# Optimization experiments

Measured on AMD Instinct MI355X. Metric: run time of the kernel, lower is better.

The kernel has to match this reference:

```python
import jax, jax.numpy as jnp
import numpy as np

D_FEAT, HID, N_LAYERS = 6, 64, 2
NEG_SLOPE = 0.01


def gru_layer(x_seq, W_ih, W_hh, b_ih, b_hh):
    # x_seq: [T, N, in]; PyTorch gate order r, z, n
    N = x_seq.shape[1]
    h0 = jnp.zeros((N, W_hh.shape[1]), x_seq.dtype)
    def step(h, x_t):
        gi = x_t @ W_ih.T + b_ih
        gh = h @ W_hh.T + b_hh
        i_r, i_z, i_n = jnp.split(gi, 3, axis=-1)
        h_r, h_z, h_n = jnp.split(gh, 3, axis=-1)
        r = jax.nn.sigmoid(i_r + h_r)
        z = jax.nn.sigmoid(i_z + h_z)
        n = jnp.tanh(i_n + r * h_n)
        h_new = (1.0 - z) * n + z * h
        return h_new, h_new
    _, ys = jax.lax.scan(step, h0, x_seq)
    return ys  # [T, N, H]


def setup_inputs() -> dict:
    key = jax.random.key(0)
    ks = jax.random.split(key, 16)
    N, T = 4000, 60
    x = jax.random.normal(ks[0], (N, D_FEAT * T), dtype=jnp.float32)
    relation_matrix = jax.random.randint(ks[1], (N, N, 8), 0, 2).astype(jnp.float32)
    s = 0.1
    p = {
        'W_ih0': jax.random.normal(ks[2], (3 * HID, D_FEAT), jnp.float32) * s,
        'W_hh0': jax.random.normal(ks[3], (3 * HID, HID), jnp.float32) * s,
        'b_ih0': jnp.zeros((3 * HID,), jnp.float32),
        'b_hh0': jnp.zeros((3 * HID,), jnp.float32),
        'W_ih1': jax.random.normal(ks[4], (3 * HID, HID), jnp.float32) * s,
        'W_hh1': jax.random.normal(ks[5], (3 * HID, HID), jnp.float32) * s,
        'b_ih1': jnp.zeros((3 * HID,), jnp.float32),
        'b_hh1': jnp.zeros((3 * HID,), jnp.float32),
        'W_0': jax.random.normal(ks[6], (2 * HID, 1), jnp.float32) * s,
        'b_0': jnp.zeros((), jnp.float32),
        'W_1': jax.random.normal(ks[7], (2 * HID, 1), jnp.float32) * s,
        'b_1': jnp.zeros((), jnp.float32),
        'W_2': jax.random.normal(ks[8], (2 * HID, 1), jnp.float32) * s,
        'b_2': jnp.zeros((), jnp.float32),
        'fc_w': jax.random.normal(ks[9], (1, 2 * HID), jnp.float32) * s,
        'fc_b': jnp.zeros((1,), jnp.float32),
    }
    return dict(x=x, relation_matrix=relation_matrix, **p)


def _head_softmax(h, W, b, mask):
    # weight[i,j] = leaky_relu(h_i @ W[:H] + h_j @ W[H:] + b); avoids [N,N,2H] concat
    H = h.shape[1]
    a = h @ W[:H]            # [N,1]
    c = h @ W[H:]            # [N,1]
    w = jax.nn.leaky_relu(a + c.T + b, NEG_SLOPE)  # [N,N]
    valid = jnp.where(mask == 0, -1000000.0, mask * w)
    return jax.nn.softmax(valid, axis=1)


def reference(x, relation_matrix, W_ih0, W_hh0, b_ih0, b_hh0, W_ih1, W_hh1, b_ih1, b_hh1,
              W_0, b_0, W_1, b_1, W_2, b_2, fc_w, fc_b):
    N = x.shape[0]
    xs = x.reshape(N, D_FEAT, -1).transpose(2, 0, 1)  # [T, N, d_feat]
    y1 = gru_layer(xs, W_ih0, W_hh0, b_ih0, b_hh0)
    y2 = gru_layer(y1, W_ih1, W_hh1, b_ih1, b_hh1)
    h = y2[-1]  # [N, H] last time step
    mask = jnp.sum(relation_matrix, axis=2)  # [N, N]
    s0 = _head_softmax(h, W_0, b_0, mask)
    s1 = _head_softmax(h, W_1, b_1, mask)
    s2 = _head_softmax(h, W_2, b_2, mask)
    agg = ((s0 + s1 + s2) / 3.0) @ h  # [N, H]
    hid = jnp.concatenate([h, agg], axis=1)  # [N, 2H]
    pred = (hid @ fc_w.T + fc_b).squeeze(-1)  # [N]
    return pred
```

## Files before the change

### kernel.cpp

```cpp
#include <hip/hip_runtime.h>

typedef __attribute__((ext_vector_type(8))) short bf16x8;
typedef __attribute__((ext_vector_type(4))) float f32x4;
typedef __attribute__((ext_vector_type(4))) float f4v;

__device__ __forceinline__ unsigned short f2bf(float f){
  unsigned u = __builtin_bit_cast(unsigned, f);
  u += 0x7FFFu + ((u >> 16) & 1u);
  return (unsigned short)(u >> 16);
}
__device__ __forceinline__ float bf2f(unsigned short b){
  unsigned u = ((unsigned)b) << 16;
  return __builtin_bit_cast(float, u);
}
__device__ __forceinline__ float sigmoidf_(float x){ return 1.f/(1.f + __expf(-x)); }
__device__ __forceinline__ float tanhf_(float x){
  float a = fabsf(x);
  float t = __expf(-2.f*a);
  float r = (1.f - t)/(1.f + t);
  return copysignf(r, x);
}

struct WF { bf16x8 hi, lo; };

__device__ __forceinline__ void mmsplit(bf16x8 ah, bf16x8 al, const WF& B,
                                        f32x4& Dh, f32x4& Dl){
  Dh = __builtin_amdgcn_mfma_f32_16x16x32_bf16(ah, B.hi, Dh, 0, 0, 0);
  Dl = __builtin_amdgcn_mfma_f32_16x16x32_bf16(al, B.hi, Dl, 0, 0, 0);
  Dl = __builtin_amdgcn_mfma_f32_16x16x32_bf16(ah, B.lo, Dl, 0, 0, 0);
}

__device__ __forceinline__ WF load_wf(const float* W, int ldk, int row, int k0, int kmax){
  WF f;
  #pragma unroll
  for (int j = 0; j < 8; j++){
    int k = k0 + j;
    float v = (k < kmax) ? W[row*ldk + k] : 0.f;
    unsigned short hb = f2bf(v);
    f.hi[j] = (short)hb;
    f.lo[j] = (short)f2bf(v - bf2f(hb));
  }
  return f;
}

__global__ __launch_bounds__(256, 1)
void gru_kernel(const float* __restrict__ x,
                const float* __restrict__ Wih0, const float* __restrict__ Whh0,
                const float* __restrict__ bih0, const float* __restrict__ bhh0,
                const float* __restrict__ Wih1, const float* __restrict__ Whh1,
                const float* __restrict__ bih1, const float* __restrict__ bhh1,
                float* __restrict__ hfin){
  __shared__ unsigned short xp_hi[16][60][8];
  __shared__ unsigned short xp_lo[16][60][8];
  __shared__ unsigned short h0hi[2][16][72], h0lo[2][16][72];
  __shared__ unsigned short h1hi[2][16][72], h1lo[2][16][72];

  const int tid  = threadIdx.x;
  const int lane = tid & 63;
  const int w    = tid >> 6;
  const int c    = lane & 15;
  const int q    = lane >> 4;
  const int d    = w*16 + c;
  const int nbase = blockIdx.x * 16;

  for (int v = tid; v < 16*360; v += 256){
    int n = v / 360, rem = v % 360;
    int dd = rem / 60, tt = rem % 60;
    float f = x[(size_t)(nbase + n)*360 + rem];
    unsigned short hb = f2bf(f);
    xp_hi[n][tt][dd] = hb;
    xp_lo[n][tt][dd] = f2bf(f - bf2f(hb));
  }
  for (int v = tid; v < 16*60*2; v += 256){
    int n = v / 120, rem = v % 120;
    int tt = rem >> 1, dd = 6 + (rem & 1);
    xp_hi[n][tt][dd] = 0; xp_lo[n][tt][dd] = 0;
  }
  for (int v = tid; v < 2*16*72; v += 256){
    ((unsigned short*)h0hi)[v] = 0; ((unsigned short*)h0lo)[v] = 0;
    ((unsigned short*)h1hi)[v] = 0; ((unsigned short*)h1lo)[v] = 0;
  }

  const float bi0r = bih0[d], bi0z = bih0[64+d], bi0n = bih0[128+d];
  const float bh0r = bhh0[d], bh0z = bhh0[64+d], bh0n = bhh0[128+d];
  const float bi1r = bih1[d], bi1z = bih1[64+d], bi1n = bih1[128+d];
  const float bh1r = bhh1[d], bh1z = bhh1[64+d], bh1n = bhh1[128+d];

  WF Bih0[3];
  WF Bhh0[3][2], Bih1[3][2], Bhh1[3][2];
  #pragma unroll
  for (int g = 0; g < 3; g++){
    int row = g*64 + d;
    Bih0[g] = load_wf(Wih0, 6, row, q*8, 6);
    #pragma unroll
    for (int kt = 0; kt < 2; kt++){
      Bhh0[g][kt] = load_wf(Whh0, 64, row, kt*32 + q*8, 64);
      Bih1[g][kt] = load_wf(Wih1, 64, row, kt*32 + q*8, 64);
      Bhh1[g][kt] = load_wf(Whh1, 64, row, kt*32 + q*8, 64);
    }
  }

  float h0old[4] = {0,0,0,0}, h1old[4] = {0,0,0,0};

  __syncthreads();

  #pragma unroll 1
  for (int t = 0; t < 60; t++){
    const int p  = t & 1;
    const int qb = p ^ 1;

    bf16x8 a_h0h[2], a_h0l[2];
    #pragma unroll
    for (int kt = 0; kt < 2; kt++){
      a_h0h[kt] = *(const bf16x8*)&h0hi[p][c][kt*32 + q*8];
      a_h0l[kt] = *(const bf16x8*)&h0lo[p][c][kt*32 + q*8];
    }
    bf16x8 a_xh = {}, a_xl = {};
    if (q == 0){
      a_xh = *(const bf16x8*)&xp_hi[c][t][0];
      a_xl = *(const bf16x8*)&xp_lo[c][t][0];
    }

    f32x4 RH = {0,0,0,0}, RL = {0,0,0,0};
    f32x4 ZH = {0,0,0,0}, ZL = {0,0,0,0};
    f32x4 NIH = {0,0,0,0}, NIL = {0,0,0,0};
    f32x4 NHH = {0,0,0,0}, NHL = {0,0,0,0};
    mmsplit(a_xh, a_xl, Bih0[0], RH, RL);
    mmsplit(a_xh, a_xl, Bih0[1], ZH, ZL);
    mmsplit(a_xh, a_xl, Bih0[2], NIH, NIL);
    #pragma unroll
    for (int kt = 0; kt < 2; kt++){
      mmsplit(a_h0h[kt], a_h0l[kt], Bhh0[0][kt], RH, RL);
      mmsplit(a_h0h[kt], a_h0l[kt], Bhh0[1][kt], ZH, ZL);
      mmsplit(a_h0h[kt], a_h0l[kt], Bhh0[2][kt], NHH, NHL);
    }
    #pragma unroll
    for (int rI = 0; rI < 4; rI++){
      float rv = sigmoidf_(RH[rI] + RL[rI] + bi0r + bh0r);
      float zv = sigmoidf_(ZH[rI] + ZL[rI] + bi0z + bh0z);
      float nv = tanhf_(NIH[rI] + NIL[rI] + bi0n + rv*(NHH[rI] + NHL[rI] + bh0n));
      float hnew = (1.f - zv)*nv + zv*h0old[rI];
      h0old[rI] = hnew;
      unsigned short hb = f2bf(hnew);
      int node = q*4 + rI;
      h0hi[qb][node][d] = hb;
      h0lo[qb][node][d] = f2bf(hnew - bf2f(hb));
    }
    __syncthreads();

    bf16x8 a_yh[2], a_yl[2], a_h1h[2], a_h1l[2];
    #pragma unroll
    for (int kt = 0; kt < 2; kt++){
      a_yh[kt]  = *(const bf16x8*)&h0hi[qb][c][kt*32 + q*8];
      a_yl[kt]  = *(const bf16x8*)&h0lo[qb][c][kt*32 + q*8];
      a_h1h[kt] = *(const bf16x8*)&h1hi[p][c][kt*32 + q*8];
      a_h1l[kt] = *(const bf16x8*)&h1lo[p][c][kt*32 + q*8];
    }
    f32x4 EH = {0,0,0,0}, EL = {0,0,0,0};
    f32x4 FH = {0,0,0,0}, FL = {0,0,0,0};
    f32x4 GIH = {0,0,0,0}, GIL = {0,0,0,0};
    f32x4 GHH = {0,0,0,0}, GHL = {0,0,0,0};
    #pragma unroll
    for (int kt = 0; kt < 2; kt++){
      mmsplit(a_yh[kt], a_yl[kt], Bih1[0][kt], EH, EL);
      mmsplit(a_yh[kt], a_yl[kt], Bih1[1][kt], FH, FL);
      mmsplit(a_yh[kt], a_yl[kt], Bih1[2][kt], GIH, GIL);
      mmsplit(a_h1h[kt], a_h1l[kt], Bhh1[0][kt], EH, EL);
      mmsplit(a_h1h[kt], a_h1l[kt], Bhh1[1][kt], FH, FL);
      mmsplit(a_h1h[kt], a_h1l[kt], Bhh1[2][kt], GHH, GHL);
    }
    #pragma unroll
    for (int rI = 0; rI < 4; rI++){
      float rv = sigmoidf_(EH[rI] + EL[rI] + bi1r + bh1r);
      float zv = sigmoidf_(FH[rI] + FL[rI] + bi1z + bh1z);
      float nv = tanhf_(GIH[rI] + GIL[rI] + bi1n + rv*(GHH[rI] + GHL[rI] + bh1n));
      float hnew = (1.f - zv)*nv + zv*h1old[rI];
      h1old[rI] = hnew;
      unsigned short hb = f2bf(hnew);
      int node = q*4 + rI;
      h1hi[qb][node][d] = hb;
      h1lo[qb][node][d] = f2bf(hnew - bf2f(hb));
    }
  }

  #pragma unroll
  for (int rI = 0; rI < 4; rI++){
    int node = nbase + q*4 + rI;
    hfin[(size_t)node*64 + d] = h1old[rI];
  }
}

__global__ void ac_kernel(const float* __restrict__ hfin,
                          const float* __restrict__ W0h, const float* __restrict__ W1h,
                          const float* __restrict__ W2h, float* __restrict__ ac){
  int lane = threadIdx.x & 63;
  int node = blockIdx.x*4 + (threadIdx.x >> 6);
  float hv = hfin[(size_t)node*64 + lane];
  const float* Ws[3] = {W0h, W1h, W2h};
  #pragma unroll
  for (int h = 0; h < 3; h++){
    float pa = hv * Ws[h][lane];
    float pc = hv * Ws[h][64 + lane];
    #pragma unroll
    for (int m = 32; m >= 1; m >>= 1){
      pa += __shfl_xor(pa, m, 64);
      pc += __shfl_xor(pc, m, 64);
    }
    if (lane == 0){
      ac[(size_t)(2*h)*4000 + node]   = pa;
      ac[(size_t)(2*h+1)*4000 + node] = pc;
    }
  }
}

__global__ __launch_bounds__(256, 3)
void attn2_kernel(const float* __restrict__ rel, const float* __restrict__ hfin,
                  const float* __restrict__ ac,
                  const float* __restrict__ b0p, const float* __restrict__ b1p,
                  const float* __restrict__ b2p,
                  const float* __restrict__ fcw, const float* __restrict__ fcb,
                  float* __restrict__ pred){
  __shared__ float m0[4000], m1[4000];
  __shared__ float red[4][8];

  const int tid  = threadIdx.x;
  const int lane = tid & 63;
  const int w    = tid >> 6;
  const int i0   = blockIdx.x * 2;
  const float bh[3] = {b0p[0], b1p[0], b2p[0]};

  const float* c0 = ac + 1*4000;
  const float* c1 = ac + 3*4000;
  const float* c2 = ac + 5*4000;

  float ai[2][3];
  #pragma unroll
  for (int r = 0; r < 2; r++)
    #pragma unroll
    for (int h = 0; h < 3; h++)
      ai[r][h] = ac[(size_t)(2*h)*4000 + i0 + r];

  float z[2][3] = {{0.f,0.f,0.f},{0.f,0.f,0.f}};

  {
    int j = tid;
    bool have = (j < 4000);
    f4v r0, r1, r2, r3;
    if (have){
      const f4v* rp0 = (const f4v*)(rel + ((size_t)i0*4000 + j)*8);
      const f4v* rp1 = (const f4v*)(rel + ((size_t)(i0+1)*4000 + j)*8);
      r0 = __builtin_nontemporal_load(rp0);
      r1 = __builtin_nontemporal_load(rp0 + 1);
      r2 = __builtin_nontemporal_load(rp1);
      r3 = __builtin_nontemporal_load(rp1 + 1);
    }
    while (have){
      int jn = j + 256;
      bool haven = (jn < 4000);
      f4v n0, n1, n2, n3;
      if (haven){
        const f4v* rp0 = (const f4v*)(rel + ((size_t)i0*4000 + jn)*8);
        const f4v* rp1 = (const f4v*)(rel + ((size_t)(i0+1)*4000 + jn)*8);
        n0 = __builtin_nontemporal_load(rp0);
        n1 = __builtin_nontemporal_load(rp0 + 1);
        n2 = __builtin_nontemporal_load(rp1);
        n3 = __builtin_nontemporal_load(rp1 + 1);
      }
      float mk0 = r0[0]+r0[1]+r0[2]+r0[3] + r1[0]+r1[1]+r1[2]+r1[3];
      float mk1 = r2[0]+r2[1]+r2[2]+r2[3] + r3[0]+r3[1]+r3[2]+r3[3];
      m0[j] = mk0; m1[j] = mk1;
      float cv[3] = {c0[j], c1[j], c2[j]};
      #pragma unroll
      for (int h = 0; h < 3; h++){
        float s0 = ai[0][h] + cv[h] + bh[h];
        float s1 = ai[1][h] + cv[h] + bh[h];
        float w0 = s0 > 0.f ? s0 : 0.01f*s0;
        float w1 = s1 > 0.f ? s1 : 0.01f*s1;
        float v0 = (mk0 == 0.f) ? -1e6f : mk0*w0;
        float v1 = (mk1 == 0.f) ? -1e6f : mk1*w1;
        z[0][h] += __expf(v0);
        z[1][h] += __expf(v1);
      }
      r0 = n0; r1 = n1; r2 = n2; r3 = n3;
      j = jn; have = haven;
    }
  }
  #pragma unroll
  for (int r = 0; r < 2; r++)
    #pragma unroll
    for (int h = 0; h < 3; h++){
      float v = z[r][h];
      #pragma unroll
      for (int m = 32; m >= 1; m >>= 1) v += __shfl_xor(v, m, 64);
      if (lane == 0) red[w][r*3 + h] = v;
    }
  __syncthreads();
  float iZ[2][3];
  #pragma unroll
  for (int r = 0; r < 2; r++)
    #pragma unroll
    for (int h = 0; h < 3; h++)
      iZ[r][h] = 1.f/(red[0][r*3+h] + red[1][r*3+h] + red[2][r*3+h] + red[3][r*3+h]);

  for (int j = tid; j < 4000; j += 256){
    float mk0 = m0[j], mk1 = m1[j];
    float cv[3] = {c0[j], c1[j], c2[j]};
    float w0s = 0.f, w1s = 0.f;
    #pragma unroll
    for (int h = 0; h < 3; h++){
      float s0 = ai[0][h] + cv[h] + bh[h];
      float s1 = ai[1][h] + cv[h] + bh[h];
      float w0 = s0 > 0.f ? s0 : 0.01f*s0;
      float w1 = s1 > 0.f ? s1 : 0.01f*s1;
      float v0 = (mk0 == 0.f) ? -1e6f : mk0*w0;
      float v1 = (mk1 == 0.f) ? -1e6f : mk1*w1;
      w0s += __expf(v0) * iZ[0][h];
      w1s += __expf(v1) * iZ[1][h];
    }
    m0[j] = w0s * (1.f/3.f);
    m1[j] = w1s * (1.f/3.f);
  }
  __syncthreads();

  float acc0 = 0.f, acc1 = 0.f;
  const int jb = w * 1000;
  for (int jj = 0; jj < 1000; jj += 4){
    float4 w0 = *(const float4*)&m0[jb + jj];
    float4 w1 = *(const float4*)&m1[jb + jj];
    float w0a[4] = {w0.x, w0.y, w0.z, w0.w};
    float w1a[4] = {w1.x, w1.y, w1.z, w1.w};
    #pragma unroll
    for (int k = 0; k < 4; k++){
      float hv = hfin[(size_t)(jb + jj + k)*64 + lane];
      acc0 = fmaf(w0a[k], hv, acc0);
      acc1 = fmaf(w1a[k], hv, acc1);
    }
  }
  __syncthreads();
  m0[(w*2 + 0)*64 + lane] = acc0;
  m0[(w*2 + 1)*64 + lane] = acc1;
  __syncthreads();
  if (tid < 128){
    int r = tid >> 6, d = tid & 63;
    float agg = m0[(0*2+r)*64 + d] + m0[(1*2+r)*64 + d]
              + m0[(2*2+r)*64 + d] + m0[(3*2+r)*64 + d];
    float term = hfin[(size_t)(i0+r)*64 + d]*fcw[d] + agg*fcw[64 + d];
    #pragma unroll
    for (int m = 32; m >= 1; m >>= 1) term += __shfl_xor(term, m, 64);
    if (d == 0) pred[i0 + r] = term + fcb[0];
  }
}

extern "C" void kernel_launch(void* const* d_in, const int* in_sizes, int n_in,
                              void* d_out, int out_size, void* d_ws, size_t ws_size,
                              hipStream_t stream) {
  const float* x    = (const float*)d_in[0];
  const float* rel  = (const float*)d_in[1];
  const float* Wih0 = (const float*)d_in[2];
  const float* Whh0 = (const float*)d_in[3];
  const float* bih0 = (const float*)d_in[4];
  const float* bhh0 = (const float*)d_in[5];
  const float* Wih1 = (const float*)d_in[6];
  const float* Whh1 = (const float*)d_in[7];
  const float* bih1 = (const float*)d_in[8];
  const float* bhh1 = (const float*)d_in[9];
  const float* W0   = (const float*)d_in[10];
  const float* b0   = (const float*)d_in[11];
  const float* W1   = (const float*)d_in[12];
  const float* b1   = (const float*)d_in[13];
  const float* W2   = (const float*)d_in[14];
  const float* b2   = (const float*)d_in[15];
  const float* fcw  = (const float*)d_in[16];
  const float* fcb  = (const float*)d_in[17];
  float* pred = (float*)d_out;
  float* hfin = (float*)d_ws;
  float* ac   = hfin + 4000*64;

  gru_kernel<<<dim3(250), dim3(256), 0, stream>>>(x, Wih0, Whh0, bih0, bhh0,
                                                  Wih1, Whh1, bih1, bhh1, hfin);
  ac_kernel<<<dim3(1000), dim3(256), 0, stream>>>(hfin, W0, W1, W2, ac);
  attn2_kernel<<<dim3(2000), dim3(256), 0, stream>>>(rel, hfin, ac, b0, b1, b2,
                                                     fcw, fcb, pred);
}
```

Measured before the change: 876.9 us.

## Specialize wavefronts per GRU layer and pipeline layer 1 one step behind

Doubles the block to 512 threads. Waves 0-3 run GRU layer 0 at step t while waves 4-7 run layer 1 at step t-1, with one barrier per step. Before, the two layers ran one after the other inside each timestep, so the critical path was the sum of both; now it is roughly the slower of the two. Each wave only holds one layer's weight fragments, but the launch bounds of (512, 2) cap registers per thread, which risks spills given the split hi/lo bf16 weight fragments and accumulators.

```diff
diff --git a/kernel.cpp b/kernel.cpp
--- a/kernel.cpp
+++ b/kernel.cpp
@@ -43,7 +43,7 @@
   return f;
 }
 
-__global__ __launch_bounds__(256, 1)
+__global__ __launch_bounds__(512, 2)
 void gru_kernel(const float* __restrict__ x,
                 const float* __restrict__ Wih0, const float* __restrict__ Whh0,
                 const float* __restrict__ bih0, const float* __restrict__ bhh0,
@@ -57,13 +57,15 @@
 
   const int tid  = threadIdx.x;
   const int lane = tid & 63;
-  const int w    = tid >> 6;
+  const int wv   = tid >> 6;
+  const bool isA = (wv < 4);
+  const int w    = wv & 3;
   const int c    = lane & 15;
   const int q    = lane >> 4;
   const int d    = w*16 + c;
   const int nbase = blockIdx.x * 16;
 
-  for (int v = tid; v < 16*360; v += 256){
+  for (int v = tid; v < 16*360; v += 512){
     int n = v / 360, rem = v % 360;
     int dd = rem / 60, tt = rem % 60;
     float f = x[(size_t)(nbase + n)*360 + rem];
@@ -71,122 +73,136 @@
     xp_hi[n][tt][dd] = hb;
     xp_lo[n][tt][dd] = f2bf(f - bf2f(hb));
   }
-  for (int v = tid; v < 16*60*2; v += 256){
+  for (int v = tid; v < 16*60*2; v += 512){
     int n = v / 120, rem = v % 120;
     int tt = rem >> 1, dd = 6 + (rem & 1);
     xp_hi[n][tt][dd] = 0; xp_lo[n][tt][dd] = 0;
   }
-  for (int v = tid; v < 2*16*72; v += 256){
+  for (int v = tid; v < 2*16*72; v += 512){
     ((unsigned short*)h0hi)[v] = 0; ((unsigned short*)h0lo)[v] = 0;
     ((unsigned short*)h1hi)[v] = 0; ((unsigned short*)h1lo)[v] = 0;
   }
 
-  const float bi0r = bih0[d], bi0z = bih0[64+d], bi0n = bih0[128+d];
-  const float bh0r = bhh0[d], bh0z = bhh0[64+d], bh0n = bhh0[128+d];
-  const float bi1r = bih1[d], bi1z = bih1[64+d], bi1n = bih1[128+d];
-  const float bh1r = bhh1[d], bh1z = bhh1[64+d], bh1n = bhh1[128+d];
-
-  WF Bih0[3];
-  WF Bhh0[3][2], Bih1[3][2], Bhh1[3][2];
+  const float* bib = isA ? bih0 : bih1;
+  const float* bhb = isA ? bhh0 : bhh1;
+  const float bir = bib[d], biz = bib[64+d], bin = bib[128+d];
+  const float bhr = bhb[d], bhz = bhb[64+d], bhn = bhb[128+d];
+
+  WF Bu[3][2], Bv[3][2];
   #pragma unroll
   for (int g = 0; g < 3; g++){
     int row = g*64 + d;
-    Bih0[g] = load_wf(Wih0, 6, row, q*8, 6);
+    if (isA){
+      Bu[g][0] = load_wf(Wih0, 6, row, q*8, 6);
+      Bu[g][1] = Bu[g][0];
+      #pragma unroll
+      for (int kt = 0; kt < 2; kt++)
+        Bv[g][kt] = load_wf(Whh0, 64, row, kt*32 + q*8, 64);
+    } else {
+      #pragma unroll
+      for (int kt = 0; kt < 2; kt++){
+        Bu[g][kt] = load_wf(Wih1, 64, row, kt*32 + q*8, 64);
+        Bv[g][kt] = load_wf(Whh1, 64, row, kt*32 + q*8, 64);
+      }
+    }
+  }
+
+  float hold[4] = {0,0,0,0};
+
+  auto stepB = [&](int s){
+    const int rb = (s + 1) & 1;
+    const int sb = s & 1;
+    bf16x8 ayh[2], ayl[2], ahh[2], ahl[2];
     #pragma unroll
     for (int kt = 0; kt < 2; kt++){
-      Bhh0[g][kt] = load_wf(Whh0, 64, row, kt*32 + q*8, 64);
-      Bih1[g][kt] = load_wf(Wih1, 64, row, kt*32 + q*8, 64);
-      Bhh1[g][kt] = load_wf(Whh1, 64, row, kt*32 + q*8, 64);
-    }
-  }
-
-  float h0old[4] = {0,0,0,0}, h1old[4] = {0,0,0,0};
-
-  __syncthreads();
-
-  #pragma unroll 1
-  for (int t = 0; t < 60; t++){
-    const int p  = t & 1;
-    const int qb = p ^ 1;
-
-    bf16x8 a_h0h[2], a_h0l[2];
-    #pragma unroll
-    for (int kt = 0; kt < 2; kt++){
-      a_h0h[kt] = *(const bf16x8*)&h0hi[p][c][kt*32 + q*8];
-      a_h0l[kt] = *(const bf16x8*)&h0lo[p][c][kt*32 + q*8];
-    }
-    bf16x8 a_xh = {}, a_xl = {};
-    if (q == 0){
-      a_xh = *(const bf16x8*)&xp_hi[c][t][0];
-      a_xl = *(const bf16x8*)&xp_lo[c][t][0];
-    }
-
+      ayh[kt] = *(const bf16x8*)&h0hi[rb][c][kt*32 + q*8];
+      ayl[kt] = *(const bf16x8*)&h0lo[rb][c][kt*32 + q*8];
+      ahh[kt] = *(const bf16x8*)&h1hi[sb][c][kt*32 + q*8];
+      ahl[kt] = *(const bf16x8*)&h1lo[sb][c][kt*32 + q*8];
+    }
     f32x4 RH = {0,0,0,0}, RL = {0,0,0,0};
     f32x4 ZH = {0,0,0,0}, ZL = {0,0,0,0};
     f32x4 NIH = {0,0,0,0}, NIL = {0,0,0,0};
     f32x4 NHH = {0,0,0,0}, NHL = {0,0,0,0};
-    mmsplit(a_xh, a_xl, Bih0[0], RH, RL);
-    mmsplit(a_xh, a_xl, Bih0[1], ZH, ZL);
-    mmsplit(a_xh, a_xl, Bih0[2], NIH, NIL);
     #pragma unroll
     for (int kt = 0; kt < 2; kt++){
-      mmsplit(a_h0h[kt], a_h0l[kt], Bhh0[0][kt], RH, RL);
-      mmsplit(a_h0h[kt], a_h0l[kt], Bhh0[1][kt], ZH, ZL);
-      mmsplit(a_h0h[kt], a_h0l[kt], Bhh0[2][kt], NHH, NHL);
+      mmsplit(ayh[kt], ayl[kt], Bu[0][kt], RH, RL);
+      mmsplit(ayh[kt], ayl[kt], Bu[1][kt], ZH, ZL);
+      mmsplit(ayh[kt], ayl[kt], Bu[2][kt], NIH, NIL);
+      mmsplit(ahh[kt], ahl[kt], Bv[0][kt], RH, RL);
+      mmsplit(ahh[kt], ahl[kt], Bv[1][kt], ZH, ZL);
+      mmsplit(ahh[kt], ahl[kt], Bv[2][kt], NHH, NHL);
     }
     #pragma unroll
     for (int rI = 0; rI < 4; rI++){
-      float rv = sigmoidf_(RH[rI] + RL[rI] + bi0r + bh0r);
-      float zv = sigmoidf_(ZH[rI] + ZL[rI] + bi0z + bh0z);
-      float nv = tanhf_(NIH[rI] + NIL[rI] + bi0n + rv*(NHH[rI] + NHL[rI] + bh0n));
-      float hnew = (1.f - zv)*nv + zv*h0old[rI];
-      h0old[rI] = hnew;
+      float rv = sigmoidf_(RH[rI] + RL[rI] + bir + bhr);
+      float zv = sigmoidf_(ZH[rI] + ZL[rI] + biz + bhz);
+      float nv = tanhf_(NIH[rI] + NIL[rI] + bin + rv*(NHH[rI] + NHL[rI] + bhn));
+      float hnew = (1.f - zv)*nv + zv*hold[rI];
+      hold[rI] = hnew;
       unsigned short hb = f2bf(hnew);
       int node = q*4 + rI;
-      h0hi[qb][node][d] = hb;
-      h0lo[qb][node][d] = f2bf(hnew - bf2f(hb));
+      h1hi[rb][node][d] = hb;
+      h1lo[rb][node][d] = f2bf(hnew - bf2f(hb));
+    }
+  };
+
+  __syncthreads();
+
+  #pragma unroll 1
+  for (int t = 0; t < 60; t++){
+    if (isA){
+      const int p  = t & 1;
+      const int nb = p ^ 1;
+      bf16x8 ah[2], al[2];
+      #pragma unroll
+      for (int kt = 0; kt < 2; kt++){
+        ah[kt] = *(const bf16x8*)&h0hi[p][c][kt*32 + q*8];
+        al[kt] = *(const bf16x8*)&h0lo[p][c][kt*32 + q*8];
+      }
+      bf16x8 axh = {}, axl = {};
+      if (q == 0){
+        axh = *(const bf16x8*)&xp_hi[c][t][0];
+        axl = *(const bf16x8*)&xp_lo[c][t][0];
+      }
+      f32x4 RH = {0,0,0,0}, RL = {0,0,0,0};
+      f32x4 ZH = {0,0,0,0}, ZL = {0,0,0,0};
+      f32x4 NIH = {0,0,0,0}, NIL = {0,0,0,0};
+      f32x4 NHH = {0,0,0,0}, NHL = {0,0,0,0};
+      mmsplit(axh, axl, Bu[0][0], RH, RL);
+      mmsplit(axh, axl, Bu[1][0], ZH, ZL);
+      mmsplit(axh, axl, Bu[2][0], NIH, NIL);
+      #pragma unroll
+      for (int kt = 0; kt < 2; kt++){
+        mmsplit(ah[kt], al[kt], Bv[0][kt], RH, RL);
+        mmsplit(ah[kt], al[kt], Bv[1][kt], ZH, ZL);
+        mmsplit(ah[kt], al[kt], Bv[2][kt], NHH, NHL);
+      }
+      #pragma unroll
+      for (int rI = 0; rI < 4; rI++){
+        float rv = sigmoidf_(RH[rI] + RL[rI] + bir + bhr);
+        float zv = sigmoidf_(ZH[rI] + ZL[rI] + biz + bhz);
+        float nv = tanhf_(NIH[rI] + NIL[rI] + bin + rv*(NHH[rI] + NHL[rI] + bhn));
+        float hnew = (1.f - zv)*nv + zv*hold[rI];
+        hold[rI] = hnew;
+        unsigned short hb = f2bf(hnew);
+        int node = q*4 + rI;
+        h0hi[nb][node][d] = hb;
+        h0lo[nb][node][d] = f2bf(hnew - bf2f(hb));
+      }
+    } else if (t > 0){
+      stepB(t - 1);
     }
     __syncthreads();
-
-    bf16x8 a_yh[2], a_yl[2], a_h1h[2], a_h1l[2];
-    #pragma unroll
-    for (int kt = 0; kt < 2; kt++){
-      a_yh[kt]  = *(const bf16x8*)&h0hi[qb][c][kt*32 + q*8];
-      a_yl[kt]  = *(const bf16x8*)&h0lo[qb][c][kt*32 + q*8];
-      a_h1h[kt] = *(const bf16x8*)&h1hi[p][c][kt*32 + q*8];
-      a_h1l[kt] = *(const bf16x8*)&h1lo[p][c][kt*32 + q*8];
-    }
-    f32x4 EH = {0,0,0,0}, EL = {0,0,0,0};
-    f32x4 FH = {0,0,0,0}, FL = {0,0,0,0};
-    f32x4 GIH = {0,0,0,0}, GIL = {0,0,0,0};
-    f32x4 GHH = {0,0,0,0}, GHL = {0,0,0,0};
-    #pragma unroll
-    for (int kt = 0; kt < 2; kt++){
-      mmsplit(a_yh[kt], a_yl[kt], Bih1[0][kt], EH, EL);
-      mmsplit(a_yh[kt], a_yl[kt], Bih1[1][kt], FH, FL);
-      mmsplit(a_yh[kt], a_yl[kt], Bih1[2][kt], GIH, GIL);
-      mmsplit(a_h1h[kt], a_h1l[kt], Bhh1[0][kt], EH, EL);
-      mmsplit(a_h1h[kt], a_h1l[kt], Bhh1[1][kt], FH, FL);
-      mmsplit(a_h1h[kt], a_h1l[kt], Bhh1[2][kt], GHH, GHL);
-    }
+  }
+
+  if (!isA){
+    stepB(59);
     #pragma unroll
     for (int rI = 0; rI < 4; rI++){
-      float rv = sigmoidf_(EH[rI] + EL[rI] + bi1r + bh1r);
-      float zv = sigmoidf_(FH[rI] + FL[rI] + bi1z + bh1z);
-      float nv = tanhf_(GIH[rI] + GIL[rI] + bi1n + rv*(GHH[rI] + GHL[rI] + bh1n));
-      float hnew = (1.f - zv)*nv + zv*h1old[rI];
-      h1old[rI] = hnew;
-      unsigned short hb = f2bf(hnew);
-      int node = q*4 + rI;
-      h1hi[qb][node][d] = hb;
-      h1lo[qb][node][d] = f2bf(hnew - bf2f(hb));
-    }
-  }
-
-  #pragma unroll
-  for (int rI = 0; rI < 4; rI++){
-    int node = nbase + q*4 + rI;
-    hfin[(size_t)node*64 + d] = h1old[rI];
+      int node = nbase + q*4 + rI;
+      hfin[(size_t)node*64 + d] = hold[rI];
+    }
   }
 }
 
@@ -376,7 +392,7 @@
   float* hfin = (float*)d_ws;
   float* ac   = hfin + 4000*64;
 
-  gru_kernel<<<dim3(250), dim3(256), 0, stream>>>(x, Wih0, Whh0, bih0, bhh0,
+  gru_kernel<<<dim3(250), dim3(512), 0, stream>>>(x, Wih0, Whh0, bih0, bhh0,
                                                   Wih1, Whh1, bih1, bhh1, hfin);
   ac_kernel<<<dim3(1000), dim3(256), 0, stream>>>(hfin, W0, W1, W2, ac);
   attn2_kernel<<<dim3(2000), dim3(256), 0, stream>>>(rel, hfin, ac, b0, b1, b2,
```

After: 862.1 us. Within noise of the previous version (-1.7%).
